# Kernel tuning notes

Measured on AMD Instinct MI355X. Metric: run time of the kernel, lower is better.

## Reference

```python
import jax, jax.numpy as jnp
import numpy as np

H = 16      # heads
DH = 64     # dim_head
EPS = 1e-6
ROPE_BASE = 10000.0


def _rms_norm(t, w):
    # torch.nn.RMSNorm over last dim (inner_dim)
    var = jnp.mean(t * t, axis=-1, keepdims=True)
    return t * jax.lax.rsqrt(var + EPS) * w


def _rope(t):
    # t: (b, n, h, d) with d split as (d/2, 2) interleaved pairs
    b, n, h, d = t.shape
    theta = 1.0 / (ROPE_BASE ** (jnp.arange(0, d, 2, dtype=jnp.float32) / d))  # (d/2,)
    pos_theta = jnp.arange(n, dtype=jnp.float32)[:, None] * theta[None, :]     # (n, d/2)
    cos = jnp.cos(pos_theta)[None, :, None, :]  # (1, n, 1, d/2)
    sin = jnp.sin(pos_theta)[None, :, None, :]
    tp = t.reshape(b, n, h, d // 2, 2)
    x0, x1 = tp[..., 0], tp[..., 1]
    r0 = cos * x0 - sin * x1
    r1 = sin * x0 + cos * x1
    return jnp.stack([r0, r1], axis=-1).reshape(b, n, h, d)


def setup_inputs() -> dict:
    key = jax.random.key(0)
    ks = jax.random.split(key, 5)
    B, N, D = 2, 2048, 1024
    inner = H * DH
    scale = 1.0 / np.sqrt(D)
    return {
        "x": jax.random.normal(ks[0], (B, N, D), dtype=jnp.float32),
        "Wq": jax.random.normal(ks[1], (D, inner), dtype=jnp.float32) * scale,
        "Wkv": jax.random.normal(ks[2], (D, 2 * inner), dtype=jnp.float32) * scale,
        "norm_q_w": jnp.ones((inner,), dtype=jnp.float32),
        "norm_k_w": jnp.ones((inner,), dtype=jnp.float32),
        "Wo": jax.random.normal(ks[3], (inner, D), dtype=jnp.float32) * scale,
        "bo": jnp.zeros((D,), dtype=jnp.float32),
    }


def reference(x, Wq, Wkv, norm_q_w, norm_k_w, Wo, bo):
    B, N, D = x.shape
    q = x @ Wq                       # (b, n, inner)
    kv = x @ Wkv                     # (b, n, 2*inner)
    k, v = jnp.split(kv, 2, axis=-1)
    q = _rms_norm(q, norm_q_w)
    k = _rms_norm(k, norm_k_w)
    # (b, n, h, d)
    q = q.reshape(B, N, H, DH)
    k = k.reshape(B, N, H, DH)
    v = v.reshape(B, N, H, DH)
    q = _rope(q)
    k = _rope(k)
    # SDPA: softmax(q k^T / sqrt(d)) v, heads as batch dim
    scores = jnp.einsum("bnhd,bmhd->bhnm", q, k) / np.sqrt(DH)
    attn = jax.nn.softmax(scores, axis=-1)
    out = jnp.einsum("bhnm,bmhd->bnhd", attn, v).reshape(B, N, H * DH)
    return out @ Wo + bo
```

## Files before the change

### kernel.cpp

```cpp
#include <hip/hip_runtime.h>

typedef __bf16 bf16;
typedef _Float16 f16;
typedef __bf16 bf16x8 __attribute__((ext_vector_type(8)));
typedef _Float16 f16x4 __attribute__((ext_vector_type(4)));
typedef _Float16 f16x8 __attribute__((ext_vector_type(8)));
typedef float f32x4 __attribute__((ext_vector_type(4)));
typedef float f32x16 __attribute__((ext_vector_type(16)));

__device__ __forceinline__ void async16(const void* g, void* l) {
  __builtin_amdgcn_global_load_lds(
      (const __attribute__((address_space(1))) unsigned int*)g,
      (__attribute__((address_space(3))) unsigned int*)l, 16, 0, 0);
}

__device__ __forceinline__ unsigned cvtpk(float a, float b) {
  unsigned r;
  asm("v_cvt_pk_bf16_f32 %0, %1, %2" : "=v"(r) : "v"(a), "v"(b));
  return r;
}

__device__ __forceinline__ void swap32(unsigned& a, unsigned& b) {
  asm("v_permlane32_swap_b32 %0, %1" : "+v"(a), "+v"(b));
}

__global__ __launch_bounds__(256) void castx(const float* __restrict__ in,
                                             f16* __restrict__ out) {
  long i = ((long)blockIdx.x * 256 + threadIdx.x) * 4;
  f32x4 v = *(const f32x4*)(in + i);
  f16x4 o;
#pragma unroll
  for (int j = 0; j < 4; j++) o[j] = (f16)v[j];
  *(f16x4*)(out + i) = o;
}

__global__ __launch_bounds__(256) void tcast(const float* __restrict__ in,
                                             f16* __restrict__ out, int R, int C) {
  __shared__ float tile[32][33];
  int tx = threadIdx.x, ty = threadIdx.y;
  int c = blockIdx.x * 32 + tx;
#pragma unroll
  for (int i = 0; i < 4; i++) {
    int r = blockIdx.y * 32 + ty + i * 8;
    tile[ty + i * 8][tx] = in[(long)r * C + c];
  }
  __syncthreads();
  int c2 = blockIdx.y * 32 + tx;
#pragma unroll
  for (int i = 0; i < 4; i++) {
    int r2 = blockIdx.x * 32 + ty + i * 8;
    out[(long)r2 * R + c2] = (f16)tile[tx][ty + i * 8];
  }
}

__global__ __launch_bounds__(256) void vtrans(const f16* __restrict__ src,
                                              bf16* __restrict__ vt) {
  __shared__ f16 tile[32][33];
  int tx = threadIdx.x, ty = threadIdx.y;
  int n0 = blockIdx.x * 32, d0 = blockIdx.y * 32, bh = blockIdx.z;
  int b = bh >> 4, h = bh & 15;
#pragma unroll
  for (int i = 0; i < 4; i++) {
    int n = n0 + ty + i * 8;
    tile[ty + i * 8][tx] = src[(long)(b * 2048 + n) * 3072 + h * 64 + d0 + tx];
  }
  __syncthreads();
#pragma unroll
  for (int i = 0; i < 4; i++) {
    int d = d0 + ty + i * 8;
    vt[((long)(bh * 64 + d)) * 2048 + n0 + tx] = (bf16)(float)tile[tx][ty + i * 8];
  }
}

template <int MODE>
__global__ __launch_bounds__(512) void gemm_f16(const f16* __restrict__ A_g,
                                                const f16* __restrict__ B_g,
                                                float* __restrict__ p0,
                                                float* __restrict__ p1,
                                                f16* __restrict__ outh,
                                                int M, int N, int K) {
  __shared__ __align__(16) f16 AL[2][4096], BL[2][4096];
  int t = threadIdx.x, lane = t & 63, w = t >> 6;
  int wm = w >> 1, wn = w & 1;
  int m0 = blockIdx.y * 128, n0 = blockIdx.x * 128;
  int fm = lane & 15, fq = lane >> 4;
  int kseg = K / gridDim.z;
  int kstart = blockIdx.z * kseg;
  int nk = kseg / 32;

  const f16* ap = A_g + (long)(m0 + w * 16 + fm) * K + kstart + fq * 8;
  const f16* bp = B_g + (long)(n0 + w * 16 + fm) * K + kstart + fq * 8;

  f32x4 acc[2][4];
#pragma unroll
  for (int i = 0; i < 2; i++)
#pragma unroll
    for (int j = 0; j < 4; j++) acc[i][j] = f32x4{0.f, 0.f, 0.f, 0.f};

  async16(ap, &AL[0][w * 512]);
  async16(bp, &BL[0][w * 512]);

  for (int it = 0; it < nk; it++) {
    int cur = it & 1;
    __syncthreads();
    if (it < nk - 1) {
      int ko = (it + 1) * 32;
      async16(ap + ko, &AL[cur ^ 1][w * 512]);
      async16(bp + ko, &BL[cur ^ 1][w * 512]);
    }
    f16x8 a[2], bfr[4];
#pragma unroll
    for (int i = 0; i < 2; i++)
      a[i] = *(const f16x8*)&AL[cur][(wm * 2 + i) * 512 + lane * 8];
#pragma unroll
    for (int j = 0; j < 4; j++)
      bfr[j] = *(const f16x8*)&BL[cur][(wn * 4 + j) * 512 + lane * 8];
#pragma unroll
    for (int i = 0; i < 2; i++)
#pragma unroll
      for (int j = 0; j < 4; j++)
        acc[i][j] = __builtin_amdgcn_mfma_f32_16x16x32_f16(a[i], bfr[j], acc[i][j], 0, 0, 0);
  }

  float* dst = blockIdx.z ? p1 : p0;
#pragma unroll
  for (int i = 0; i < 2; i++)
#pragma unroll
    for (int j = 0; j < 4; j++) {
      int c = n0 + (wn * 4 + j) * 16 + fm;
#pragma unroll
      for (int e = 0; e < 4; e++) {
        int r = m0 + (wm * 2 + i) * 16 + fq * 4 + e;
        if (MODE == 0)
          dst[(long)r * N + c] = acc[i][j][e];
        else
          outh[(long)r * N + c] = (f16)acc[i][j][e];
      }
    }
}

__global__ __launch_bounds__(256) void addbias(const float* __restrict__ p0,
                                               const float* __restrict__ p1,
                                               const float* __restrict__ bias,
                                               float* __restrict__ out) {
  long i = ((long)blockIdx.x * 256 + threadIdx.x) * 4;
  f32x4 a = *(const f32x4*)(p0 + i);
  f32x4 b = *(const f32x4*)(p1 + i);
  f32x4 c = *(const f32x4*)(bias + (i & 1023));
  *(f32x4*)(out + i) = a + b + c;
}

__global__ __launch_bounds__(256) void normrope(const f16* __restrict__ src,
                                                const float* __restrict__ wqn,
                                                const float* __restrict__ wkn,
                                                f16* __restrict__ qf,
                                                f16* __restrict__ kf) {
  int row = blockIdx.x, which = blockIdx.y;
  const f16* sp = src + (long)row * 3072 + which * 1024;
  const float* w = which ? wkn : wqn;
  f16* oh = which ? kf : qf;
  float scale = which ? 1.0f : 0.125f;
  int t = threadIdx.x;
  int j0 = t * 4;

  f16x4 xh = *(const f16x4*)(sp + j0);
  float xv[4];
#pragma unroll
  for (int j = 0; j < 4; j++) xv[j] = (float)xh[j];
  float ss = xv[0] * xv[0] + xv[1] * xv[1] + xv[2] * xv[2] + xv[3] * xv[3];
#pragma unroll
  for (int off = 32; off > 0; off >>= 1) ss += __shfl_down(ss, off);
  __shared__ float red[4];
  if ((t & 63) == 0) red[t >> 6] = ss;
  __syncthreads();
  float total = red[0] + red[1] + red[2] + red[3];
  float nsc = rsqrtf(total * (1.0f / 1024.0f) + 1e-6f) * scale;

  int n = row & 2047;
  f16x4 o;
#pragma unroll
  for (int pp = 0; pp < 2; pp++) {
    int j = j0 + 2 * pp;
    int ii = (j & 63) >> 1;
    float theta = __expf((float)ii * (-9.210340371976184f / 32.0f));
    float ang = (float)n * theta;
    float sn, cs;
    __sincosf(ang, &sn, &cs);
    float a0 = xv[2 * pp] * nsc * w[j];
    float a1 = xv[2 * pp + 1] * nsc * w[j + 1];
    o[2 * pp] = (f16)(cs * a0 - sn * a1);
    o[2 * pp + 1] = (f16)(sn * a0 + cs * a1);
  }
  *(f16x4*)(oh + (long)row * 1024 + j0) = o;
}

__global__ __launch_bounds__(256) void attn_mfma(const f16* __restrict__ qf,
                                                 const f16* __restrict__ kf,
                                                 const bf16* __restrict__ vt,
                                                 f16* __restrict__ pO,
                                                 float* __restrict__ pl) {
  __shared__ __align__(16) f16 KhL[2][4096];
  __shared__ __align__(16) bf16 VtL[2][4096];

  int t = threadIdx.x;
  int lane = t & 63, w = t >> 6;
  int lo5 = lane & 31, hi = lane >> 5;
  int z = blockIdx.z;
  int b = z >> 1, ksp = z & 1;
  int h = blockIdx.y, q0 = blockIdx.x * 128;

  const f16* qb = qf + ((long)(b * 2048 + q0 + w * 32 + lo5)) * 1024 + h * 64 + hi * 8;
  f16x8 qfr[4];
#pragma unroll
  for (int ks = 0; ks < 4; ks++) qfr[ks] = *(const f16x8*)(qb + ks * 16);

  int r8 = lane >> 3;
  int ch = (lane & 7) ^ r8;
  const char* kgb = (const char*)(kf + ((long)(b * 2048)) * 1024 + h * 64);
  const char* vgb = (const char*)(vt + ((long)((b * 16 + h) * 64)) * 2048);

  int koff[4];
#pragma unroll
  for (int ks = 0; ks < 4; ks++)
    koff[ks] = lo5 * 128 + ((ks * 32 + hi * 16) ^ ((lane & 7) << 4));

  f32x16 Ot[2];
#pragma unroll
  for (int i = 0; i < 16; i++) {
    Ot[0][i] = 0.f;
    Ot[1][i] = 0.f;
  }
  float l_ = 0.f;

  int kb0 = ksp * 16;

#define STAGE(buf, kb)                                                        \
  {                                                                           \
    _Pragma("unroll") for (int uu = 0; uu < 2; uu++) {                        \
      int u = w * 2 + uu;                                                     \
      async16(kgb + ((long)((kb) * 64 + u * 8 + r8)) * 2048 + ch * 16,        \
              (char*)KhL[buf] + u * 1024);                                    \
      async16(vgb + ((long)(u * 8 + r8)) * 4096 + (long)(kb) * 128 + ch * 16, \
              (char*)VtL[buf] + u * 1024);                                    \
    }                                                                         \
  }

  STAGE(0, kb0);

  for (int it = 0; it < 16; it++) {
    int cur = it & 1;
    __syncthreads();
    if (it < 15) STAGE(cur ^ 1, kb0 + it + 1);

    const char* kbase = (const char*)KhL[cur];
    const char* vbase = (const char*)VtL[cur];

    f32x16 s0, s1;
#pragma unroll
    for (int i = 0; i < 16; i++) {
      s0[i] = 0.f;
      s1[i] = 0.f;
    }
#pragma unroll
    for (int ks = 0; ks < 4; ks++) {
      f16x8 k0 = *(const f16x8*)(kbase + koff[ks]);
      f16x8 k1 = *(const f16x8*)(kbase + 4096 + koff[ks]);
      s0 = __builtin_amdgcn_mfma_f32_32x32x16_f16(k0, qfr[ks], s0, 0, 0, 0);
      s1 = __builtin_amdgcn_mfma_f32_32x32x16_f16(k1, qfr[ks], s1, 0, 0, 0);
    }

    union PF {
      unsigned u[4];
      bf16x8 v;
    } pf[4];
#pragma unroll
    for (int nt = 0; nt < 2; nt++) {
      f32x16 s = nt ? s1 : s0;
      float pv[16];
#pragma unroll
      for (int r = 0; r < 16; r++) {
        pv[r] = __expf(s[r]);
        l_ += pv[r];
      }
#pragma unroll
      for (int g = 0; g < 2; g++) {
        unsigned c01 = cvtpk(pv[g * 8 + 0], pv[g * 8 + 1]);
        unsigned c23 = cvtpk(pv[g * 8 + 2], pv[g * 8 + 3]);
        unsigned c45 = cvtpk(pv[g * 8 + 4], pv[g * 8 + 5]);
        unsigned c67 = cvtpk(pv[g * 8 + 6], pv[g * 8 + 7]);
        swap32(c01, c45);
        swap32(c23, c67);
        pf[nt * 2 + g].u[0] = c01;
        pf[nt * 2 + g].u[1] = c23;
        pf[nt * 2 + g].u[2] = c45;
        pf[nt * 2 + g].u[3] = c67;
      }
    }

#pragma unroll
    for (int ks = 0; ks < 4; ks++) {
      bf16x8 v0 = *(const bf16x8*)(vbase + koff[ks]);
      bf16x8 v1 = *(const bf16x8*)(vbase + 4096 + koff[ks]);
      Ot[0] = __builtin_amdgcn_mfma_f32_32x32x16_bf16(v0, pf[ks].v, Ot[0], 0, 0, 0);
      Ot[1] = __builtin_amdgcn_mfma_f32_32x32x16_bf16(v1, pf[ks].v, Ot[1], 0, 0, 0);
    }
  }
#undef STAGE

  l_ += __shfl_xor(l_, 32);
  float inv = 1.0f / l_;

  long rowi = ((long)((ksp * 2 + b) * 16 + h)) * 2048 + q0 + w * 32 + lo5;
  f16* op = pO + rowi * 64;
#pragma unroll
  for (int dt = 0; dt < 2; dt++)
#pragma unroll
    for (int g4 = 0; g4 < 4; g4++) {
      f16x4 o4;
#pragma unroll
      for (int e = 0; e < 4; e++) o4[e] = (f16)(Ot[dt][g4 * 4 + e] * inv);
      *(f16x4*)(op + dt * 32 + g4 * 8 + hi * 4) = o4;
    }
  if (hi == 0) pl[rowi] = l_;
}

__global__ __launch_bounds__(256) void attn_combine(const f16* __restrict__ pO,
                                                    const float* __restrict__ pl,
                                                    f16* __restrict__ af) {
  int dg = threadIdx.x & 15;
  int qi = threadIdx.x >> 4;
  int q = blockIdx.x * 16 + qi;
  int h = blockIdx.y, b = blockIdx.z;
  long r0 = ((long)(b * 16 + h)) * 2048 + q;
  long r1 = ((long)((2 + b) * 16 + h)) * 2048 + q;
  float l0 = pl[r0], l1 = pl[r1];
  float w0 = l0 / (l0 + l1), w1 = 1.0f - w0;
  f16x4 a = *(const f16x4*)(pO + r0 * 64 + dg * 4);
  f16x4 c = *(const f16x4*)(pO + r1 * 64 + dg * 4);
  f16x4 o;
#pragma unroll
  for (int e = 0; e < 4; e++) o[e] = (f16)((float)a[e] * w0 + (float)c[e] * w1);
  *(f16x4*)(af + ((long)(b * 2048 + q)) * 1024 + h * 64 + dg * 4) = o;
}

extern "C" void kernel_launch(void* const* d_in, const int* in_sizes, int n_in,
                              void* d_out, int out_size, void* d_ws, size_t ws_size,
                              hipStream_t stream) {
  const float* x = (const float*)d_in[0];
  const float* Wq = (const float*)d_in[1];
  const float* Wkv = (const float*)d_in[2];
  const float* nqw = (const float*)d_in[3];
  const float* nkw = (const float*)d_in[4];
  const float* Wo = (const float*)d_in[5];
  const float* bo = (const float*)d_in[6];
  float* out = (float*)d_out;

  char* ws = (char*)d_ws;
  const long MB = 1l << 20;
  f16* xf     = (f16*)(ws);
  f16* Wqkv_t = (f16*)(ws + 8 * MB);
  f16* qkv_f  = (f16*)(ws + 14 * MB);
  f16* qfb    = (f16*)(ws + 38 * MB);
  f16* kfb    = (f16*)(ws + 46 * MB);
  bf16* vtb   = (bf16*)(ws + 54 * MB);
  f16* pOb    = (f16*)(ws + 14 * MB);
  float* plb  = (float*)(ws + 30 * MB);
  f16* afb    = (f16*)(ws);
  f16* Wo_t   = (f16*)(ws + 8 * MB);
  float* p0   = (float*)(ws + 14 * MB);
  float* p1   = (float*)(ws + 30 * MB);

  dim3 tb(32, 8);
  castx<<<4096, 256, 0, stream>>>(x, xf);
  tcast<<<dim3(32, 32), tb, 0, stream>>>(Wq, Wqkv_t, 1024, 1024);
  tcast<<<dim3(64, 32), tb, 0, stream>>>(Wkv, Wqkv_t + 1024l * 1024, 1024, 2048);

  gemm_f16<1><<<dim3(24, 32), 512, 0, stream>>>(xf, Wqkv_t, nullptr, nullptr,
                                                qkv_f, 4096, 3072, 1024);

  normrope<<<dim3(4096, 2), 256, 0, stream>>>(qkv_f, nqw, nkw, qfb, kfb);

  vtrans<<<dim3(64, 2, 32), tb, 0, stream>>>(qkv_f + 2048, vtb);

  attn_mfma<<<dim3(16, 16, 4), 256, 0, stream>>>(qfb, kfb, vtb, pOb, plb);

  attn_combine<<<dim3(128, 16, 2), 256, 0, stream>>>(pOb, plb, afb);

  tcast<<<dim3(32, 32), tb, 0, stream>>>(Wo, Wo_t, 1024, 1024);

  gemm_f16<0><<<dim3(8, 32, 2), 512, 0, stream>>>(afb, Wo_t, p0, p1, nullptr,
                                                  4096, 1024, 1024);

  addbias<<<4096, 256, 0, stream>>>(p0, p1, bo, out);
}
```

Baseline: 250.7 us.

## Pre-swizzle K and V^T into MFMA fragment order for contiguous attention loads

The normrope and vtrans kernels now write K and transposed V directly in a per-(batch,head) blocked layout that matches the MFMA operand fragment order. The attention kernel can then stage each 64-key block with four fully contiguous async16 loads per wave, and read LDS fragments at lane*16 offsets without XOR swizzle address arithmetic. This is meant to cut global-load scatter and address computation in the attention loop. In exchange, the producer kernels do more scattered stores, and the plain lane-linear LDS reads could cause bank conflicts.

Result: no change. 252.4 us (+0.7%).

```diff
diff --git a/kernel.cpp b/kernel.cpp
--- a/kernel.cpp
+++ b/kernel.cpp
@@ -54,7 +54,7 @@
 }
 
 __global__ __launch_bounds__(256) void vtrans(const f16* __restrict__ src,
-                                              bf16* __restrict__ vt) {
+                                              bf16* __restrict__ vtf) {
   __shared__ f16 tile[32][33];
   int tx = threadIdx.x, ty = threadIdx.y;
   int n0 = blockIdx.x * 32, d0 = blockIdx.y * 32, bh = blockIdx.z;
@@ -68,7 +68,10 @@
 #pragma unroll
   for (int i = 0; i < 4; i++) {
     int d = d0 + ty + i * 8;
-    vt[((long)(bh * 64 + d)) * 2048 + n0 + tx] = (bf16)(float)tile[tx][ty + i * 8];
+    int n = n0 + tx;
+    long off = ((((long)bh * 32 + (n >> 6)) * 8 + (d >> 5) * 4 + ((n & 63) >> 4)) * 64 +
+                ((n >> 3) & 1) * 32 + (d & 31)) * 8 + (n & 7);
+    vtf[off] = (bf16)(float)tile[tx][ty + i * 8];
   }
 }
 
@@ -154,11 +157,10 @@
                                                 const float* __restrict__ wqn,
                                                 const float* __restrict__ wkn,
                                                 f16* __restrict__ qf,
-                                                f16* __restrict__ kf) {
+                                                f16* __restrict__ kff) {
   int row = blockIdx.x, which = blockIdx.y;
   const f16* sp = src + (long)row * 3072 + which * 1024;
   const float* w = which ? wkn : wqn;
-  f16* oh = which ? kf : qf;
   float scale = which ? 1.0f : 0.125f;
   int t = threadIdx.x;
   int j0 = t * 4;
@@ -191,12 +193,20 @@
     o[2 * pp] = (f16)(cs * a0 - sn * a1);
     o[2 * pp + 1] = (f16)(sn * a0 + cs * a1);
   }
-  *(f16x4*)(oh + (long)row * 1024 + j0) = o;
+  if (which == 0) {
+    *(f16x4*)(qf + (long)row * 1024 + j0) = o;
+  } else {
+    int b2 = row >> 11;
+    int h2 = j0 >> 6, dl = j0 & 63;
+    long off = ((((long)(b2 * 16 + h2) * 32 + (n >> 6)) * 8 + ((n >> 5) & 1) * 4 +
+                 (dl >> 4)) * 64 + ((dl >> 3) & 1) * 32 + (n & 31)) * 8 + (dl & 7);
+    *(f16x4*)(kff + off) = o;
+  }
 }
 
 __global__ __launch_bounds__(256) void attn_mfma(const f16* __restrict__ qf,
-                                                 const f16* __restrict__ kf,
-                                                 const bf16* __restrict__ vt,
+                                                 const f16* __restrict__ kff,
+                                                 const bf16* __restrict__ vtf,
                                                  f16* __restrict__ pO,
                                                  float* __restrict__ pl) {
   __shared__ __align__(16) f16 KhL[2][4096];
@@ -214,15 +224,8 @@
 #pragma unroll
   for (int ks = 0; ks < 4; ks++) qfr[ks] = *(const f16x8*)(qb + ks * 16);
 
-  int r8 = lane >> 3;
-  int ch = (lane & 7) ^ r8;
-  const char* kgb = (const char*)(kf + ((long)(b * 2048)) * 1024 + h * 64);
-  const char* vgb = (const char*)(vt + ((long)((b * 16 + h) * 64)) * 2048);
-
-  int koff[4];
-#pragma unroll
-  for (int ks = 0; ks < 4; ks++)
-    koff[ks] = lo5 * 128 + ((ks * 32 + hi * 16) ^ ((lane & 7) << 4));
+  const f16* kg = kff + ((long)(b * 16 + h)) * 131072 + (2 * w) * 512 + lane * 8;
+  const bf16* vg = vtf + ((long)(b * 16 + h)) * 131072 + (2 * w) * 512 + lane * 8;
 
   f32x16 Ot[2];
 #pragma unroll
@@ -234,15 +237,14 @@
 
   int kb0 = ksp * 16;
 
-#define STAGE(buf, kb)                                                        \
-  {                                                                           \
-    _Pragma("unroll") for (int uu = 0; uu < 2; uu++) {                        \
-      int u = w * 2 + uu;                                                     \
-      async16(kgb + ((long)((kb) * 64 + u * 8 + r8)) * 2048 + ch * 16,        \
-              (char*)KhL[buf] + u * 1024);                                    \
-      async16(vgb + ((long)(u * 8 + r8)) * 4096 + (long)(kb) * 128 + ch * 16, \
-              (char*)VtL[buf] + u * 1024);                                    \
-    }                                                                         \
+#define STAGE(buf, kb)                                                     \
+  {                                                                        \
+    async16(kg + (long)(kb) * 4096, (char*)KhL[buf] + (2 * w) * 1024);     \
+    async16(kg + (long)(kb) * 4096 + 512,                                  \
+            (char*)KhL[buf] + (2 * w + 1) * 1024);                         \
+    async16(vg + (long)(kb) * 4096, (char*)VtL[buf] + (2 * w) * 1024);     \
+    async16(vg + (long)(kb) * 4096 + 512,                                  \
+            (char*)VtL[buf] + (2 * w + 1) * 1024);                         \
   }
 
   STAGE(0, kb0);
@@ -263,8 +265,8 @@
     }
 #pragma unroll
     for (int ks = 0; ks < 4; ks++) {
-      f16x8 k0 = *(const f16x8*)(kbase + koff[ks]);
-      f16x8 k1 = *(const f16x8*)(kbase + 4096 + koff[ks]);
+      f16x8 k0 = *(const f16x8*)(kbase + ks * 1024 + (long)lane * 16);
+      f16x8 k1 = *(const f16x8*)(kbase + (4 + ks) * 1024 + (long)lane * 16);
       s0 = __builtin_amdgcn_mfma_f32_32x32x16_f16(k0, qfr[ks], s0, 0, 0, 0);
       s1 = __builtin_amdgcn_mfma_f32_32x32x16_f16(k1, qfr[ks], s1, 0, 0, 0);
     }
@@ -299,8 +301,8 @@
 
 #pragma unroll
     for (int ks = 0; ks < 4; ks++) {
-      bf16x8 v0 = *(const bf16x8*)(vbase + koff[ks]);
-      bf16x8 v1 = *(const bf16x8*)(vbase + 4096 + koff[ks]);
+      bf16x8 v0 = *(const bf16x8*)(vbase + ks * 1024 + (long)lane * 16);
+      bf16x8 v1 = *(const bf16x8*)(vbase + (4 + ks) * 1024 + (long)lane * 16);
       Ot[0] = __builtin_amdgcn_mfma_f32_32x32x16_bf16(v0, pf[ks].v, Ot[0], 0, 0, 0);
       Ot[1] = __builtin_amdgcn_mfma_f32_32x32x16_bf16(v1, pf[ks].v, Ot[1], 0, 0, 0);
     }
@@ -361,8 +363,8 @@
   f16* Wqkv_t = (f16*)(ws + 8 * MB);
   f16* qkv_f  = (f16*)(ws + 14 * MB);
   f16* qfb    = (f16*)(ws + 38 * MB);
-  f16* kfb    = (f16*)(ws + 46 * MB);
-  bf16* vtb   = (bf16*)(ws + 54 * MB);
+  f16* kffb   = (f16*)(ws + 46 * MB);
+  bf16* vtfb  = (bf16*)(ws + 54 * MB);
   f16* pOb    = (f16*)(ws + 14 * MB);
   float* plb  = (float*)(ws + 30 * MB);
   f16* afb    = (f16*)(ws);
@@ -378,11 +380,11 @@
   gemm_f16<1><<<dim3(24, 32), 512, 0, stream>>>(xf, Wqkv_t, nullptr, nullptr,
                                                 qkv_f, 4096, 3072, 1024);
 
-  normrope<<<dim3(4096, 2), 256, 0, stream>>>(qkv_f, nqw, nkw, qfb, kfb);
-
-  vtrans<<<dim3(64, 2, 32), tb, 0, stream>>>(qkv_f + 2048, vtb);
-
-  attn_mfma<<<dim3(16, 16, 4), 256, 0, stream>>>(qfb, kfb, vtb, pOb, plb);
+  normrope<<<dim3(4096, 2), 256, 0, stream>>>(qkv_f, nqw, nkw, qfb, kffb);
+
+  vtrans<<<dim3(64, 2, 32), tb, 0, stream>>>(qkv_f + 2048, vtfb);
+
+  attn_mfma<<<dim3(16, 16, 4), 256, 0, stream>>>(qfb, kffb, vtfb, pOb, plb);
 
   attn_combine<<<dim3(128, 16, 2), 256, 0, stream>>>(pOb, plb, afb);
 
```
